# Kernel optimization log

Measured on AMD Instinct MI355X. Metric: run time of the kernel, lower is better.

Reference implementation:

```python
import jax, jax.numpy as jnp
import numpy as np

MU = 0.25  # commitment weight

def setup_inputs() -> dict:
    key = jax.random.key(0)
    k1, k2 = jax.random.split(key)
    x = jax.random.normal(k1, (32, 4096, 32), dtype=jnp.float32)
    codebook = jax.random.normal(k2, (256, 32), dtype=jnp.float32)
    return {"x": x, "codebook": codebook}

def reference(x, codebook):
    B, T, D = x.shape
    K = codebook.shape[0]
    xf = x.reshape(-1, D)  # [N, D]
    d2 = (jnp.sum(xf * xf, axis=-1, keepdims=True)
          + jnp.sum(codebook * codebook, axis=-1)[None, :]
          - 2.0 * (xf @ codebook.T))
    logits = -d2
    probs = jax.nn.softmax(logits, axis=-1)          # [N, K]
    indices = jnp.argmax(logits, axis=-1)            # [N]
    quants_hard = codebook[indices]                  # gather [N, D]
    commitment = jnp.mean((jax.lax.stop_gradient(quants_hard) - xf) ** 2, axis=-1)
    codebook_loss = jnp.mean((quants_hard - jax.lax.stop_gradient(xf)) ** 2, axis=-1)
    loss = codebook_loss + MU * commitment           # [N]
    quants = jax.lax.stop_gradient(quants_hard - xf) + xf  # straight-through
    return (indices.reshape(B, T),
            probs.reshape(B, T, K),
            quants.reshape(B, T, D),
            loss.reshape(B, T))
```

## Files before the change

### kernel.cpp

```cpp
#include <hip/hip_runtime.h>
#include <math.h>

constexpr int D    = 32;
constexpr int K    = 256;
constexpr int ROWS = 64;
constexpr int WPB  = 8;
constexpr int CPT  = 32;

__global__ __launch_bounds__(512, 4) void vq_kernel(
    const float* __restrict__ x,
    const float* __restrict__ cb,
    float* __restrict__ o_idx,
    float* __restrict__ o_probs,
    float* __restrict__ o_quants,
    float* __restrict__ o_loss)
{
    __shared__ __align__(16) char smem_u[40960];
    __shared__ float mred[WPB][ROWS];
    __shared__ float sred[WPB][ROWS];
    __shared__ int   ired[WPB][ROWS];

    float*  cbl  = reinterpret_cast<float*>(smem_u);
    float*  cnl  = reinterpret_cast<float*>(smem_u + 32768);
    float4* pbuf = reinterpret_cast<float4*>(smem_u);

    const int tid = threadIdx.x;
    const int l   = tid & 63;
    const int w   = tid >> 6;
    const int row = blockIdx.x * ROWS + l;

    {
        const float4* cg = reinterpret_cast<const float4*>(cb);
        float4*       cl = reinterpret_cast<float4*>(cbl);
        #pragma unroll
        for (int i = 0; i < 4; ++i) cl[tid + i * 512] = cg[tid + i * 512];
    }
    {
        const int c = tid >> 1, h = tid & 1;
        const float4* p = reinterpret_cast<const float4*>(cb) + c * (D / 4) + h * 4;
        float a = 0.f;
        #pragma unroll
        for (int i = 0; i < 4; ++i) {
            float4 v = p[i];
            a += v.x * v.x + v.y * v.y + v.z * v.z + v.w * v.w;
        }
        a += __shfl_xor(a, 1);
        if (h == 0) cnl[c] = a;
    }

    float xr[D];
    {
        const float4* xv = reinterpret_cast<const float4*>(x) + (size_t)row * (D / 4);
        #pragma unroll
        for (int i = 0; i < D / 4; ++i) {
            float4 v = xv[i];
            xr[4 * i + 0] = v.x; xr[4 * i + 1] = v.y;
            xr[4 * i + 2] = v.z; xr[4 * i + 3] = v.w;
        }
    }
    float xx;
    {
        float a0 = 0.f, a1 = 0.f, a2 = 0.f, a3 = 0.f;
        #pragma unroll
        for (int j = 0; j < D; j += 4) {
            a0 += xr[j] * xr[j];         a1 += xr[j + 1] * xr[j + 1];
            a2 += xr[j + 2] * xr[j + 2]; a3 += xr[j + 3] * xr[j + 3];
        }
        xx = (a0 + a1) + (a2 + a3);
    }
    __syncthreads();

    const int kbase = w * CPT;
    const float4* cwl = reinterpret_cast<const float4*>(cbl) + kbase * (D / 4);
    float lg[CPT];
    #pragma unroll
    for (int j = 0; j < CPT; ++j) {
        float d0 = 0.f, d1 = 0.f, d2 = 0.f, d3 = 0.f;
        #pragma unroll
        for (int t = 0; t < D / 4; ++t) {
            float4 c4 = cwl[j * (D / 4) + t];
            d0 += xr[4 * t + 0] * c4.x; d1 += xr[4 * t + 1] * c4.y;
            d2 += xr[4 * t + 2] * c4.z; d3 += xr[4 * t + 3] * c4.w;
        }
        float dot = (d0 + d1) + (d2 + d3);
        lg[j] = 2.0f * dot - (xx + cnl[kbase + j]);
    }

    float m = lg[0]; int bi = 0;
    #pragma unroll
    for (int j = 1; j < CPT; ++j) {
        bool gt = lg[j] > m;
        m  = gt ? lg[j] : m;
        bi = gt ? j : bi;
    }
    mred[w][l] = m;
    ired[w][l] = kbase + bi;
    __syncthreads();

    float gm = mred[0][l]; int gi = ired[0][l];
    #pragma unroll
    for (int ww = 1; ww < WPB; ++ww) {
        float mw = mred[ww][l];
        bool gt  = mw > gm;
        gi = gt ? ired[ww][l] : gi;
        gm = gt ? mw : gm;
    }

    float s = 0.f;
    #pragma unroll
    for (int j = 0; j < CPT; ++j) {
        float e = __expf(lg[j] - gm);
        lg[j] = e;
        s += e;
    }
    sred[w][l] = s;
    __syncthreads();

    float gs = 0.f;
    #pragma unroll
    for (int ww = 0; ww < WPB; ++ww) gs += sred[ww][l];
    const float rs = 1.0f / gs;

    if (w == 4) {
        o_idx[row] = (float)gi;
    } else if (w == 5) {
        o_loss[row] = gm * (-1.25f / (float)D);
    } else if (w >= 6) {
        const int half = w - 6;
        const float4* cg = reinterpret_cast<const float4*>(cb) + gi * (D / 4) + half * 4;
        float4* qv = reinterpret_cast<float4*>(o_quants) + (size_t)row * (D / 4) + half * 4;
        #pragma unroll
        for (int i = 0; i < 4; ++i) qv[i] = cg[i];
    }

    float4* op = reinterpret_cast<float4*>(o_probs);
    const int rowbase = blockIdx.x * ROWS;
    #pragma unroll
    for (int h = 0; h < 2; ++h) {
        float4* pb = pbuf + ((size_t)w * ROWS + l) * 5;
        #pragma unroll
        for (int i = 0; i < 4; ++i) {
            int j = h * 16 + i * 4;
            pb[i] = make_float4(lg[j] * rs, lg[j + 1] * rs,
                                lg[j + 2] * rs, lg[j + 3] * rs);
        }
        #pragma unroll
        for (int i = 0; i < 4; ++i) {
            int e  = i * 64 + l;
            int r  = e >> 2;
            int c4 = e & 3;
            float4 v = pbuf[((size_t)w * ROWS + r) * 5 + c4];
            op[(size_t)(rowbase + r) * (K / 4) + w * 8 + h * 4 + c4] = v;
        }
    }
}

extern "C" void kernel_launch(void* const* d_in, const int* in_sizes, int n_in,
                              void* d_out, int out_size, void* d_ws, size_t ws_size,
                              hipStream_t stream) {
    const float* x  = (const float*)d_in[0];
    const float* cb = (const float*)d_in[1];
    const int N = in_sizes[0] / D;

    float* out      = (float*)d_out;
    float* o_idx    = out;
    float* o_probs  = o_idx + N;
    float* o_quants = o_probs + (size_t)N * K;
    float* o_loss   = o_quants + (size_t)N * D;

    const int grid = N / ROWS;
    vq_kernel<<<grid, 512, 0, stream>>>(x, cb, o_idx, o_probs, o_quants, o_loss);
}
```

Measured before the change: 193.7 us.

## Process two rows per thread to reuse codebook LDS loads

Each thread now handles two input rows, so every codebook float4 read from shared memory feeds two dot products. Each block covers twice as many rows, which halves the number of blocks and the per-block codebook staging. Launch bounds drop to 2 blocks per CU to make room for the larger register footprint. The probability staging buffer is reused for the second row without a barrier between the writes and the cross-lane reads, which relies on each wave touching only its own region.

Result: slower. 209.3 us (+8.0%).

```diff
diff --git a/kernel.cpp b/kernel.cpp
--- a/kernel.cpp
+++ b/kernel.cpp
@@ -3,11 +3,13 @@
 
 constexpr int D    = 32;
 constexpr int K    = 256;
-constexpr int ROWS = 64;
+constexpr int LPW  = 64;
 constexpr int WPB  = 8;
 constexpr int CPT  = 32;
-
-__global__ __launch_bounds__(512, 4) void vq_kernel(
+constexpr int RPT  = 2;
+constexpr int ROWS = LPW * RPT;
+
+__global__ __launch_bounds__(512, 2) void vq_kernel(
     const float* __restrict__ x,
     const float* __restrict__ cb,
     float* __restrict__ o_idx,
@@ -16,9 +18,9 @@
     float* __restrict__ o_loss)
 {
     __shared__ __align__(16) char smem_u[40960];
-    __shared__ float mred[WPB][ROWS];
-    __shared__ float sred[WPB][ROWS];
-    __shared__ int   ired[WPB][ROWS];
+    __shared__ float mred[WPB][RPT][LPW];
+    __shared__ float sred[WPB][RPT][LPW];
+    __shared__ int   ired[WPB][RPT][LPW];
 
     float*  cbl  = reinterpret_cast<float*>(smem_u);
     float*  cnl  = reinterpret_cast<float*>(smem_u + 32768);
@@ -27,7 +29,8 @@
     const int tid = threadIdx.x;
     const int l   = tid & 63;
     const int w   = tid >> 6;
-    const int row = blockIdx.x * ROWS + l;
+    const int row0 = blockIdx.x * ROWS + l;
+    const int row1 = row0 + LPW;
 
     {
         const float4* cg = reinterpret_cast<const float4*>(cb);
@@ -48,111 +51,164 @@
         if (h == 0) cnl[c] = a;
     }
 
-    float xr[D];
-    {
-        const float4* xv = reinterpret_cast<const float4*>(x) + (size_t)row * (D / 4);
+    float xr0[D], xr1[D];
+    {
+        const float4* xv0 = reinterpret_cast<const float4*>(x) + (size_t)row0 * (D / 4);
+        const float4* xv1 = reinterpret_cast<const float4*>(x) + (size_t)row1 * (D / 4);
         #pragma unroll
         for (int i = 0; i < D / 4; ++i) {
-            float4 v = xv[i];
-            xr[4 * i + 0] = v.x; xr[4 * i + 1] = v.y;
-            xr[4 * i + 2] = v.z; xr[4 * i + 3] = v.w;
-        }
-    }
-    float xx;
+            float4 v = xv0[i];
+            xr0[4 * i + 0] = v.x; xr0[4 * i + 1] = v.y;
+            xr0[4 * i + 2] = v.z; xr0[4 * i + 3] = v.w;
+        }
+        #pragma unroll
+        for (int i = 0; i < D / 4; ++i) {
+            float4 v = xv1[i];
+            xr1[4 * i + 0] = v.x; xr1[4 * i + 1] = v.y;
+            xr1[4 * i + 2] = v.z; xr1[4 * i + 3] = v.w;
+        }
+    }
+    float xx0, xx1;
     {
         float a0 = 0.f, a1 = 0.f, a2 = 0.f, a3 = 0.f;
         #pragma unroll
         for (int j = 0; j < D; j += 4) {
-            a0 += xr[j] * xr[j];         a1 += xr[j + 1] * xr[j + 1];
-            a2 += xr[j + 2] * xr[j + 2]; a3 += xr[j + 3] * xr[j + 3];
-        }
-        xx = (a0 + a1) + (a2 + a3);
+            a0 += xr0[j] * xr0[j];         a1 += xr0[j + 1] * xr0[j + 1];
+            a2 += xr0[j + 2] * xr0[j + 2]; a3 += xr0[j + 3] * xr0[j + 3];
+        }
+        xx0 = (a0 + a1) + (a2 + a3);
+        a0 = a1 = a2 = a3 = 0.f;
+        #pragma unroll
+        for (int j = 0; j < D; j += 4) {
+            a0 += xr1[j] * xr1[j];         a1 += xr1[j + 1] * xr1[j + 1];
+            a2 += xr1[j + 2] * xr1[j + 2]; a3 += xr1[j + 3] * xr1[j + 3];
+        }
+        xx1 = (a0 + a1) + (a2 + a3);
     }
     __syncthreads();
 
     const int kbase = w * CPT;
     const float4* cwl = reinterpret_cast<const float4*>(cbl) + kbase * (D / 4);
-    float lg[CPT];
+    float lg0[CPT], lg1[CPT];
     #pragma unroll
     for (int j = 0; j < CPT; ++j) {
-        float d0 = 0.f, d1 = 0.f, d2 = 0.f, d3 = 0.f;
+        float a0 = 0.f, a1 = 0.f, a2 = 0.f, a3 = 0.f;
+        float b0 = 0.f, b1 = 0.f, b2 = 0.f, b3 = 0.f;
         #pragma unroll
         for (int t = 0; t < D / 4; ++t) {
             float4 c4 = cwl[j * (D / 4) + t];
-            d0 += xr[4 * t + 0] * c4.x; d1 += xr[4 * t + 1] * c4.y;
-            d2 += xr[4 * t + 2] * c4.z; d3 += xr[4 * t + 3] * c4.w;
-        }
-        float dot = (d0 + d1) + (d2 + d3);
-        lg[j] = 2.0f * dot - (xx + cnl[kbase + j]);
-    }
-
-    float m = lg[0]; int bi = 0;
-    #pragma unroll
-    for (int j = 1; j < CPT; ++j) {
-        bool gt = lg[j] > m;
-        m  = gt ? lg[j] : m;
-        bi = gt ? j : bi;
-    }
-    mred[w][l] = m;
-    ired[w][l] = kbase + bi;
+            a0 += xr0[4 * t + 0] * c4.x; a1 += xr0[4 * t + 1] * c4.y;
+            a2 += xr0[4 * t + 2] * c4.z; a3 += xr0[4 * t + 3] * c4.w;
+            b0 += xr1[4 * t + 0] * c4.x; b1 += xr1[4 * t + 1] * c4.y;
+            b2 += xr1[4 * t + 2] * c4.z; b3 += xr1[4 * t + 3] * c4.w;
+        }
+        const float cn = cnl[kbase + j];
+        lg0[j] = 2.0f * ((a0 + a1) + (a2 + a3)) - (xx0 + cn);
+        lg1[j] = 2.0f * ((b0 + b1) + (b2 + b3)) - (xx1 + cn);
+    }
+
+    {
+        float m = lg0[0]; int bi = 0;
+        #pragma unroll
+        for (int j = 1; j < CPT; ++j) {
+            bool gt = lg0[j] > m;
+            m  = gt ? lg0[j] : m;
+            bi = gt ? j : bi;
+        }
+        mred[w][0][l] = m;
+        ired[w][0][l] = kbase + bi;
+    }
+    {
+        float m = lg1[0]; int bi = 0;
+        #pragma unroll
+        for (int j = 1; j < CPT; ++j) {
+            bool gt = lg1[j] > m;
+            m  = gt ? lg1[j] : m;
+            bi = gt ? j : bi;
+        }
+        mred[w][1][l] = m;
+        ired[w][1][l] = kbase + bi;
+    }
     __syncthreads();
 
-    float gm = mred[0][l]; int gi = ired[0][l];
+    float gm0 = mred[0][0][l]; int gi0 = ired[0][0][l];
+    float gm1 = mred[0][1][l]; int gi1 = ired[0][1][l];
     #pragma unroll
     for (int ww = 1; ww < WPB; ++ww) {
-        float mw = mred[ww][l];
-        bool gt  = mw > gm;
-        gi = gt ? ired[ww][l] : gi;
-        gm = gt ? mw : gm;
-    }
-
-    float s = 0.f;
+        float mw0 = mred[ww][0][l];
+        bool gt0  = mw0 > gm0;
+        gi0 = gt0 ? ired[ww][0][l] : gi0;
+        gm0 = gt0 ? mw0 : gm0;
+        float mw1 = mred[ww][1][l];
+        bool gt1  = mw1 > gm1;
+        gi1 = gt1 ? ired[ww][1][l] : gi1;
+        gm1 = gt1 ? mw1 : gm1;
+    }
+
+    {
+        float s0 = 0.f, s1 = 0.f;
+        #pragma unroll
+        for (int j = 0; j < CPT; ++j) {
+            float e0 = __expf(lg0[j] - gm0);
+            float e1 = __expf(lg1[j] - gm1);
+            lg0[j] = e0; lg1[j] = e1;
+            s0 += e0; s1 += e1;
+        }
+        sred[w][0][l] = s0;
+        sred[w][1][l] = s1;
+    }
+    __syncthreads();
+
+    float gs0 = 0.f, gs1 = 0.f;
     #pragma unroll
-    for (int j = 0; j < CPT; ++j) {
-        float e = __expf(lg[j] - gm);
-        lg[j] = e;
-        s += e;
-    }
-    sred[w][l] = s;
-    __syncthreads();
-
-    float gs = 0.f;
-    #pragma unroll
-    for (int ww = 0; ww < WPB; ++ww) gs += sred[ww][l];
-    const float rs = 1.0f / gs;
+    for (int ww = 0; ww < WPB; ++ww) {
+        gs0 += sred[ww][0][l];
+        gs1 += sred[ww][1][l];
+    }
+    const float rs0 = 1.0f / gs0;
+    const float rs1 = 1.0f / gs1;
 
     if (w == 4) {
-        o_idx[row] = (float)gi;
+        o_idx[row0] = (float)gi0;
+        o_idx[row1] = (float)gi1;
     } else if (w == 5) {
-        o_loss[row] = gm * (-1.25f / (float)D);
-    } else if (w >= 6) {
-        const int half = w - 6;
-        const float4* cg = reinterpret_cast<const float4*>(cb) + gi * (D / 4) + half * 4;
-        float4* qv = reinterpret_cast<float4*>(o_quants) + (size_t)row * (D / 4) + half * 4;
-        #pragma unroll
-        for (int i = 0; i < 4; ++i) qv[i] = cg[i];
+        o_loss[row0] = gm0 * (-1.25f / (float)D);
+        o_loss[row1] = gm1 * (-1.25f / (float)D);
+    } else if (w == 6) {
+        const float4* cg = reinterpret_cast<const float4*>(cb) + gi0 * (D / 4);
+        float4* qv = reinterpret_cast<float4*>(o_quants) + (size_t)row0 * (D / 4);
+        #pragma unroll
+        for (int i = 0; i < D / 4; ++i) qv[i] = cg[i];
+    } else if (w == 7) {
+        const float4* cg = reinterpret_cast<const float4*>(cb) + gi1 * (D / 4);
+        float4* qv = reinterpret_cast<float4*>(o_quants) + (size_t)row1 * (D / 4);
+        #pragma unroll
+        for (int i = 0; i < D / 4; ++i) qv[i] = cg[i];
     }
 
     float4* op = reinterpret_cast<float4*>(o_probs);
-    const int rowbase = blockIdx.x * ROWS;
-    #pragma unroll
-    for (int h = 0; h < 2; ++h) {
-        float4* pb = pbuf + ((size_t)w * ROWS + l) * 5;
-        #pragma unroll
-        for (int i = 0; i < 4; ++i) {
-            int j = h * 16 + i * 4;
-            pb[i] = make_float4(lg[j] * rs, lg[j + 1] * rs,
-                                lg[j + 2] * rs, lg[j + 3] * rs);
-        }
-        #pragma unroll
-        for (int i = 0; i < 4; ++i) {
-            int e  = i * 64 + l;
-            int r  = e >> 2;
-            int c4 = e & 3;
-            float4 v = pbuf[((size_t)w * ROWS + r) * 5 + c4];
-            op[(size_t)(rowbase + r) * (K / 4) + w * 8 + h * 4 + c4] = v;
-        }
-    }
+    auto emit_probs = [&](const float (&lgv)[CPT], float rsv, int rowbase) {
+        #pragma unroll
+        for (int h = 0; h < 2; ++h) {
+            float4* pb = pbuf + ((size_t)w * LPW + l) * 5;
+            #pragma unroll
+            for (int i = 0; i < 4; ++i) {
+                int j = h * 16 + i * 4;
+                pb[i] = make_float4(lgv[j] * rsv, lgv[j + 1] * rsv,
+                                    lgv[j + 2] * rsv, lgv[j + 3] * rsv);
+            }
+            #pragma unroll
+            for (int i = 0; i < 4; ++i) {
+                int e  = i * 64 + l;
+                int r  = e >> 2;
+                int c4 = e & 3;
+                float4 v = pbuf[((size_t)w * LPW + r) * 5 + c4];
+                op[(size_t)(rowbase + r) * (K / 4) + w * 8 + h * 4 + c4] = v;
+            }
+        }
+    };
+    emit_probs(lg0, rs0, blockIdx.x * ROWS);
+    emit_probs(lg1, rs1, blockIdx.x * ROWS + LPW);
 }
 
 extern "C" void kernel_launch(void* const* d_in, const int* in_sizes, int n_in,
```
